# Kernel tuning notes

Hardware: AMD Instinct MI355X
Metric: run time of the kernel (lower is better)

The kernel has to match this reference:

```python
import jax, jax.numpy as jnp
import numpy as np

NUM_EMBEDDINGS = 4096
EMBEDDING_DIM = 256
COMMITMENT_COST = 0.25
N_TOKENS = 32768


def setup_inputs() -> dict:
    key = jax.random.key(0)
    k1, k2 = jax.random.split(key)
    inputs = jax.random.normal(k1, (N_TOKENS, EMBEDDING_DIM), dtype=jnp.float32)
    # torch init: uniform(-1/K, 1/K)
    lim = 1.0 / NUM_EMBEDDINGS
    weight = jax.random.uniform(k2, (NUM_EMBEDDINGS, EMBEDDING_DIM), dtype=jnp.float32,
                                minval=-lim, maxval=lim)
    return {"inputs": inputs, "weight": weight}


def reference(inputs, weight):
    distances = (jnp.sum(inputs ** 2, axis=1, keepdims=True)
                 + jnp.sum(weight ** 2, axis=1)
                 - 2.0 * jnp.matmul(inputs, weight.T))
    encoding_indices = jnp.argmin(distances, axis=1)                       # [N]
    encodings = jax.nn.one_hot(encoding_indices, NUM_EMBEDDINGS,
                               dtype=jnp.float32)                          # [N, K]
    # gather replaces onehot @ weight (same values)
    quantized = weight[encoding_indices]                                   # [N, D]

    commitment_loss = jnp.mean((jax.lax.stop_gradient(quantized) - inputs) ** 2)
    codebook_loss = jnp.mean((quantized - jax.lax.stop_gradient(inputs)) ** 2)
    loss = codebook_loss + COMMITMENT_COST * commitment_loss

    # straight-through estimator
    quantized_st = inputs + jax.lax.stop_gradient(quantized - inputs)

    avg_probs = jnp.mean(encodings, axis=0)                                # [K]
    perplexity = jnp.exp(-jnp.sum(avg_probs * jnp.log(avg_probs + 1e-10)))

    return (quantized_st, perplexity, encodings, encoding_indices, loss)
```

## Files before the change

### kernel.cpp

```cpp
#include <hip/hip_runtime.h>

#define N_TOK 32768
#define N_EMB 4096
#define DIM 256

typedef short bf16x8 __attribute__((ext_vector_type(8)));
typedef float f32x4 __attribute__((ext_vector_type(4)));
typedef unsigned short us8 __attribute__((ext_vector_type(8)));


static __device__ __forceinline__ unsigned short f2bf(float f) {
    unsigned int u = __float_as_uint(f);
    u = (u + 0x7fffu + ((u >> 16) & 1u)) >> 16;
    return (unsigned short)u;
}

__device__ __forceinline__ float pw128_sq(const float4* a4) {
#pragma clang fp contract(off)
    float4 v0 = a4[0], v1 = a4[1];
    float r0 = v0.x * v0.x, r1 = v0.y * v0.y, r2 = v0.z * v0.z, r3 = v0.w * v0.w;
    float r4 = v1.x * v1.x, r5 = v1.y * v1.y, r6 = v1.z * v1.z, r7 = v1.w * v1.w;
    #pragma unroll
    for (int i = 1; i < 16; ++i) {
        v0 = a4[2 * i]; v1 = a4[2 * i + 1];
        float s;
        s = v0.x * v0.x; r0 += s;
        s = v0.y * v0.y; r1 += s;
        s = v0.z * v0.z; r2 += s;
        s = v0.w * v0.w; r3 += s;
        s = v1.x * v1.x; r4 += s;
        s = v1.y * v1.y; r5 += s;
        s = v1.z * v1.z; r6 += s;
        s = v1.w * v1.w; r7 += s;
    }
    return ((r0 + r1) + (r2 + r3)) + ((r4 + r5) + (r6 + r7));
}

__global__ __launch_bounds__(256) void k_norm_np(const float* __restrict__ src,
                                                 float* __restrict__ dst, int nrows) {
#pragma clang fp contract(off)
    int row = blockIdx.x * 256 + threadIdx.x;
    if (row >= nrows) return;
    const float4* a = (const float4*)(src + (size_t)row * DIM);
    float lo = pw128_sq(a);
    float hi = pw128_sq(a + 32);
    dst[row] = lo + hi;
}

__global__ __launch_bounds__(256) void k_shuf1(const float* __restrict__ src,
                                               unsigned short* __restrict__ hi) {
    int tid = blockIdx.x * 256 + threadIdx.x;
    int b = tid >> 6, lane = tid & 63;
    int T = b >> 3, C = b & 7;
    int row = T * 16 + (lane & 15);
    int col = C * 32 + (lane >> 4) * 8;
    const float* s = src + (size_t)row * DIM + col;
    us8 h;
    #pragma unroll
    for (int j = 0; j < 8; ++j) h[j] = f2bf(s[j]);
    *(us8*)(hi + (size_t)tid * 8) = h;
}

__global__ __launch_bounds__(256, 4) void k_score_mfma(
        const float* __restrict__ x, const float* __restrict__ w,
        const float* __restrict__ e2_np, const float* __restrict__ x2_np,
        const unsigned short* __restrict__ Xh,
        const unsigned short* __restrict__ Wh,
        float* __restrict__ out_idx, unsigned int* __restrict__ counts,
        float* enc,
        float* __restrict__ outq, float* __restrict__ loss_acc) {
    __shared__ __align__(16) short Abuf[8192];
    __shared__ float Tmax[4][32];
    __shared__ unsigned int ccnt[32];
    __shared__ int clist[32][16];
    __shared__ float Red_d[32 * 8];
    __shared__ int   Red_i[32 * 8];
    __shared__ float sred[4];

    const int t = threadIdx.x;
    const int wave = t >> 6, lane = t & 63;
    const int tok0 = blockIdx.x * 32;
    const int q = lane >> 4, c = lane & 15;

    #pragma unroll
    for (int i = 0; i < 4; ++i) {
        int idx = wave * 4 + i;
        int tile = idx >> 3, C = idx & 7;
        int Tg = blockIdx.x * 2 + tile;
        const unsigned short* src = Xh + ((size_t)(Tg * 8 + C) * 64 + lane) * 8;
        __builtin_amdgcn_global_load_lds(
            (const __attribute__((address_space(1))) unsigned int*)src,
            (__attribute__((address_space(3))) unsigned int*)(Abuf + idx * 512),
            16, 0, 0);
    }
    if (t < 32) ccnt[t] = 0;
    __syncthreads();

    f32x4* ez = enc ? (f32x4*)(enc + (size_t)tok0 * N_EMB) : (f32x4*)0;
    const f32x4 zf4 = {0.f, 0.f, 0.f, 0.f};

    float vmax[8], v2[8];
    #pragma unroll
    for (int s = 0; s < 8; ++s) { vmax[s] = -3.4e38f; v2[s] = -3.4e38f; }
    for (int jt = 0; jt < N_EMB; jt += 256) {
        const int U0 = (jt >> 4) + wave * 4;
        f32x4 acc[2][4] = {};
        #pragma unroll
        for (int C = 0; C < 8; ++C) {
            bf16x8 ah[2], bh[4];
            #pragma unroll
            for (int m = 0; m < 2; ++m)
                ah[m] = *(const bf16x8*)(Abuf + (size_t)(m * 8 + C) * 512 + lane * 8);
            #pragma unroll
            for (int n = 0; n < 4; ++n)
                bh[n] = *(const bf16x8*)(Wh + (((size_t)(U0 + n) * 8 + C) * 64 + lane) * 8);
            #pragma unroll
            for (int m = 0; m < 2; ++m)
                #pragma unroll
                for (int n = 0; n < 4; ++n)
                    acc[m][n] = __builtin_amdgcn_mfma_f32_16x16x32_bf16(ah[m], bh[n], acc[m][n], 0, 0, 0);
        }
        {
            unsigned int idb = ((unsigned int)jt >> 8) << 2;
            #pragma unroll
            for (int m = 0; m < 2; ++m)
                #pragma unroll
                for (int n = 0; n < 4; ++n)
                    #pragma unroll
                    for (int r = 0; r < 4; ++r) {
                        float p = __uint_as_float(
                            (__float_as_uint(acc[m][n][r]) & ~63u) | (idb + (unsigned)n));
                        int s = m * 4 + r;
                        if (p > vmax[s]) { v2[s] = vmax[s]; vmax[s] = p; }
                        else if (p > v2[s]) v2[s] = p;
                    }
        }
        if (ez) {
            int base = (jt >> 8) * 8 * 256 + t;
            #pragma unroll
            for (int j = 0; j < 8; ++j)
                __builtin_nontemporal_store(zf4, ez + base + j * 256);
        }
    }
    float rmax[8];
    #pragma unroll
    for (int s = 0; s < 8; ++s) rmax[s] = vmax[s];
    #pragma unroll
    for (int off = 1; off < 16; off <<= 1)
        #pragma unroll
        for (int s = 0; s < 8; ++s)
            rmax[s] = fmaxf(rmax[s], __shfl_xor(rmax[s], off));
    if (c == 0) {
        #pragma unroll
        for (int m = 0; m < 2; ++m)
            #pragma unroll
            for (int r = 0; r < 4; ++r)
                Tmax[wave][m * 16 + q * 4 + r] = rmax[m * 4 + r];
    }
    __syncthreads();
    if (t < 32) {
        float mx = fmaxf(fmaxf(Tmax[0][t], Tmax[1][t]),
                         fmaxf(Tmax[2][t], Tmax[3][t]));
        Tmax[0][t] = mx - 1.5e-4f;
    }
    __syncthreads();
    float thr[8];
    #pragma unroll
    for (int m = 0; m < 2; ++m)
        #pragma unroll
        for (int r = 0; r < 4; ++r)
            thr[m * 4 + r] = Tmax[0][m * 16 + q * 4 + r];

    #pragma unroll
    for (int s = 0; s < 8; ++s) {
        int m = s >> 2, r = s & 3;
        int tokl = m * 16 + q * 4 + r;
        #pragma unroll
        for (int h = 0; h < 2; ++h) {
            float pv = h ? v2[s] : vmax[s];
            if (pv >= thr[s]) {
                unsigned int id = __float_as_uint(pv) & 63u;
                int code = ((int)(id >> 2) * 16 + wave * 4 + (int)(id & 3u)) * 16 + c;
                unsigned int p = atomicAdd(&ccnt[tokl], 1u);
                if (p < 16) clist[tokl][p] = code;
            }
        }
    }
    __syncthreads();

    {
        int token = t >> 3, slot = t & 7;
        int cnt = (int)ccnt[token]; if (cnt > 16) cnt = 16;
        float bd = 3.4e38f;
        int bi = 0x7fffffff;
        float x2 = x2_np[tok0 + token];
        const float4* xr = (const float4*)(x + (size_t)(tok0 + token) * DIM);
        for (int k = slot; k < cnt; k += 8) {
            int code = clist[token][k];
            const float4* wr = (const float4*)(w + (size_t)code * DIM);
            double dot = 0.0;
            for (int g = 0; g < 64; ++g) {
                float4 xv = xr[g];
                float4 wv = wr[g];
                dot += (double)xv.x * (double)wv.x;
                dot += (double)xv.y * (double)wv.y;
                dot += (double)xv.z * (double)wv.z;
                dot += (double)xv.w * (double)wv.w;
            }
            {
#pragma clang fp contract(off)
                float M  = (float)dot;
                float S  = x2 + e2_np[code];
                float dd = S - 2.0f * M;
                if (dd < bd || (dd == bd && code < bi)) { bd = dd; bi = code; }
            }
        }
        Red_d[token * 8 + slot] = bd;
        Red_i[token * 8 + slot] = bi;
    }
    __syncthreads();
    if (t < 32) {
        float fv = Red_d[t * 8];
        int   fi = Red_i[t * 8];
        #pragma unroll
        for (int k = 1; k < 8; ++k) {
            float v = Red_d[t * 8 + k];
            int  ii = Red_i[t * 8 + k];
            if (v < fv || (v == fv && ii < fi)) { fv = v; fi = ii; }
        }
        out_idx[tok0 + t] = (float)fi;
        atomicAdd(&counts[fi], 1u);
        ccnt[t] = (unsigned int)fi;
    }
    __syncthreads();

    {
        int token = t >> 3, slot = t & 7;
        int fi = (int)ccnt[token];
        if (enc && slot == 0)
            __builtin_nontemporal_store(1.0f, enc + (size_t)(tok0 + token) * N_EMB + fi);
        const f32x4* wr = (const f32x4*)(w + (size_t)fi * DIM);
        const f32x4* xr = (const f32x4*)(x + (size_t)(tok0 + token) * DIM);
        f32x4* oq = (f32x4*)(outq + (size_t)(tok0 + token) * DIM);
        float sse = 0.f;
        #pragma unroll
        for (int g0 = 0; g0 < 8; ++g0) {
            int g = slot * 8 + g0;
            f32x4 qv = wr[g];
            f32x4 xv = xr[g];
            __builtin_nontemporal_store(qv, oq + g);
            float dx = qv.x - xv.x, dy = qv.y - xv.y;
            float dz = qv.z - xv.z, dw = qv.w - xv.w;
            sse += dx * dx + dy * dy + dz * dz + dw * dw;
        }
        #pragma unroll
        for (int off = 32; off > 0; off >>= 1) sse += __shfl_down(sse, off, 64);
        if (lane == 0) sred[wave] = sse;
    }
    __syncthreads();
    if (t == 0)
        atomicAdd(loss_acc, sred[0] + sred[1] + sred[2] + sred[3]);
}

__global__ __launch_bounds__(256) void k_onehot(const float* __restrict__ out_idx,
                                                float* __restrict__ enc) {
    int token = blockIdx.x;
    int idx = (int)out_idx[token];
    float4* row = (float4*)(enc + (size_t)token * N_EMB);
    #pragma unroll
    for (int p = 0; p < 4; ++p) {
        int g = threadIdx.x + 256 * p;
        float4 v = make_float4(0.f, 0.f, 0.f, 0.f);
        int d0 = g * 4;
        if (idx >= d0 && idx < d0 + 4) ((float*)&v)[idx - d0] = 1.0f;
        row[g] = v;
    }
}

__global__ __launch_bounds__(256) void k_final(const unsigned int* __restrict__ counts,
                                               const float* __restrict__ loss_acc,
                                               float* __restrict__ out_perp,
                                               float* __restrict__ out_loss) {
    __shared__ float sred[4];
    int t = threadIdx.x;
    float h = 0.f;
    for (int k = t; k < N_EMB; k += 256) {
        float p = (float)counts[k] * (1.0f / N_TOK);
        h += p * logf(p + 1e-10f);
    }
    #pragma unroll
    for (int off = 32; off > 0; off >>= 1) h += __shfl_down(h, off, 64);
    if ((t & 63) == 0) sred[t >> 6] = h;
    __syncthreads();
    if (t == 0) {
        float s = sred[0] + sred[1] + sred[2] + sred[3];
        *out_perp = expf(-s);
        *out_loss = loss_acc[0] * 1.25f / 8388608.0f;
    }
}

extern "C" void kernel_launch(void* const* d_in, const int* in_sizes, int n_in,
                              void* d_out, int out_size, void* d_ws, size_t ws_size,
                              hipStream_t stream) {
    const float* x = (const float*)d_in[0];
    const float* w = (const float*)d_in[1];
    float* out  = (float*)d_out;
    float* out0 = out;
    float* out1 = out0 + 8388608;
    float* out2 = out1 + 1;
    float* out3 = out2 + 134217728;
    float* out4 = out3 + 32768;

    unsigned int* counts = (unsigned int*)d_ws;
    float* loss_acc = (float*)((char*)d_ws + 16384);
    float* e2_np    = (float*)((char*)d_ws + 16896);
    float* x2_np    = (float*)((char*)d_ws + 33280);

    bool big_ws = ws_size >= (size_t)(20u * 1024u * 1024u);
    unsigned short *Xh, *Wh;
    float* enc_arg;
    if (big_ws) {
        Xh = (unsigned short*)((char*)d_ws + (1u << 20));
        Wh = Xh + 8388608;
        enc_arg = out2;
    } else {
        uintptr_t sb = ((uintptr_t)out2 + 255) & ~(uintptr_t)255;
        Xh = (unsigned short*)sb;
        Wh = Xh + 8388608;
        enc_arg = nullptr;
    }

    hipMemsetAsync(d_ws, 0, 16640, stream);
    k_norm_np<<<N_EMB / 256, 256, 0, stream>>>(w, e2_np, N_EMB);
    k_norm_np<<<N_TOK / 256, 256, 0, stream>>>(x, x2_np, N_TOK);
    k_shuf1<<<N_TOK * DIM / 8 / 256, 256, 0, stream>>>(x, Xh);
    k_shuf1<<<N_EMB * DIM / 8 / 256, 256, 0, stream>>>(w, Wh);
    k_score_mfma<<<N_TOK / 32, 256, 0, stream>>>(x, w, e2_np, x2_np, Xh, Wh,
                                                 out3, counts, enc_arg,
                                                 out0, loss_acc);
    if (!big_ws)
        k_onehot<<<N_TOK, 256, 0, stream>>>(out3, out2);
    k_final<<<1, 256, 0, stream>>>(counts, loss_acc, out1, out4);
}
```

Measured before the change: 756.5 us.

## Double token tile per block and use branchless top-2 tracking

Each scoring block now handles 64 tokens instead of 32, so every W fragment loaded from global memory feeds four MFMAs instead of two. This halves the total codebook traffic across the grid. The top-2 tracking after each MFMA tile is rewritten with fmax/fmed3 instead of branches, processing four candidates at a time. In exchange the accumulators and top-2 state double, which raises register pressure (launch bounds lowered to 3 waves), halves the grid, and gives fewer threads per token in the refinement and output phases.

```diff
diff --git a/kernel.cpp b/kernel.cpp
--- a/kernel.cpp
+++ b/kernel.cpp
@@ -13,6 +13,10 @@
     unsigned int u = __float_as_uint(f);
     u = (u + 0x7fffu + ((u >> 16) & 1u)) >> 16;
     return (unsigned short)u;
+}
+
+static __device__ __forceinline__ float pkid(float x, unsigned int id) {
+    return __uint_as_float((__float_as_uint(x) & ~63u) | id);
 }
 
 __device__ __forceinline__ float pw128_sq(const float4* a4) {
@@ -61,7 +65,7 @@
     *(us8*)(hi + (size_t)tid * 8) = h;
 }
 
-__global__ __launch_bounds__(256, 4) void k_score_mfma(
+__global__ __launch_bounds__(256, 3) void k_score_mfma(
         const float* __restrict__ x, const float* __restrict__ w,
         const float* __restrict__ e2_np, const float* __restrict__ x2_np,
         const unsigned short* __restrict__ Xh,
@@ -69,110 +73,113 @@
         float* __restrict__ out_idx, unsigned int* __restrict__ counts,
         float* enc,
         float* __restrict__ outq, float* __restrict__ loss_acc) {
-    __shared__ __align__(16) short Abuf[8192];
-    __shared__ float Tmax[4][32];
-    __shared__ unsigned int ccnt[32];
-    __shared__ int clist[32][16];
-    __shared__ float Red_d[32 * 8];
-    __shared__ int   Red_i[32 * 8];
+    __shared__ __align__(16) short Abuf[16384];
+    __shared__ float Tmax[4][64];
+    __shared__ unsigned int ccnt[64];
+    __shared__ int clist[64][16];
+    __shared__ float Red_d[64 * 4];
+    __shared__ int   Red_i[64 * 4];
     __shared__ float sred[4];
 
     const int t = threadIdx.x;
     const int wave = t >> 6, lane = t & 63;
-    const int tok0 = blockIdx.x * 32;
+    const int tok0 = blockIdx.x * 64;
     const int q = lane >> 4, c = lane & 15;
 
     #pragma unroll
-    for (int i = 0; i < 4; ++i) {
-        int idx = wave * 4 + i;
+    for (int i = 0; i < 8; ++i) {
+        int idx = wave * 8 + i;
         int tile = idx >> 3, C = idx & 7;
-        int Tg = blockIdx.x * 2 + tile;
+        int Tg = blockIdx.x * 4 + tile;
         const unsigned short* src = Xh + ((size_t)(Tg * 8 + C) * 64 + lane) * 8;
         __builtin_amdgcn_global_load_lds(
             (const __attribute__((address_space(1))) unsigned int*)src,
             (__attribute__((address_space(3))) unsigned int*)(Abuf + idx * 512),
             16, 0, 0);
     }
-    if (t < 32) ccnt[t] = 0;
+    if (t < 64) ccnt[t] = 0;
     __syncthreads();
 
     f32x4* ez = enc ? (f32x4*)(enc + (size_t)tok0 * N_EMB) : (f32x4*)0;
     const f32x4 zf4 = {0.f, 0.f, 0.f, 0.f};
 
-    float vmax[8], v2[8];
-    #pragma unroll
-    for (int s = 0; s < 8; ++s) { vmax[s] = -3.4e38f; v2[s] = -3.4e38f; }
+    float vmax[16], v2[16];
+    #pragma unroll
+    for (int s = 0; s < 16; ++s) { vmax[s] = -3.4e38f; v2[s] = -3.4e38f; }
     for (int jt = 0; jt < N_EMB; jt += 256) {
         const int U0 = (jt >> 4) + wave * 4;
-        f32x4 acc[2][4] = {};
+        f32x4 acc[4][4] = {};
         #pragma unroll
         for (int C = 0; C < 8; ++C) {
-            bf16x8 ah[2], bh[4];
-            #pragma unroll
-            for (int m = 0; m < 2; ++m)
+            bf16x8 ah[4];
+            #pragma unroll
+            for (int m = 0; m < 4; ++m)
                 ah[m] = *(const bf16x8*)(Abuf + (size_t)(m * 8 + C) * 512 + lane * 8);
             #pragma unroll
-            for (int n = 0; n < 4; ++n)
-                bh[n] = *(const bf16x8*)(Wh + (((size_t)(U0 + n) * 8 + C) * 64 + lane) * 8);
-            #pragma unroll
-            for (int m = 0; m < 2; ++m)
+            for (int n = 0; n < 4; ++n) {
+                bf16x8 bh = *(const bf16x8*)(Wh + (((size_t)(U0 + n) * 8 + C) * 64 + lane) * 8);
                 #pragma unroll
-                for (int n = 0; n < 4; ++n)
-                    acc[m][n] = __builtin_amdgcn_mfma_f32_16x16x32_bf16(ah[m], bh[n], acc[m][n], 0, 0, 0);
+                for (int m = 0; m < 4; ++m)
+                    acc[m][n] = __builtin_amdgcn_mfma_f32_16x16x32_bf16(ah[m], bh, acc[m][n], 0, 0, 0);
+            }
         }
         {
             unsigned int idb = ((unsigned int)jt >> 8) << 2;
             #pragma unroll
-            for (int m = 0; m < 2; ++m)
+            for (int m = 0; m < 4; ++m)
                 #pragma unroll
-                for (int n = 0; n < 4; ++n)
-                    #pragma unroll
-                    for (int r = 0; r < 4; ++r) {
-                        float p = __uint_as_float(
-                            (__float_as_uint(acc[m][n][r]) & ~63u) | (idb + (unsigned)n));
-                        int s = m * 4 + r;
-                        if (p > vmax[s]) { v2[s] = vmax[s]; vmax[s] = p; }
-                        else if (p > v2[s]) v2[s] = p;
-                    }
+                for (int r = 0; r < 4; ++r) {
+                    int s = m * 4 + r;
+                    float p0 = pkid(acc[m][0][r], idb + 0);
+                    float p1 = pkid(acc[m][1][r], idb + 1);
+                    float p2 = pkid(acc[m][2][r], idb + 2);
+                    float p3 = pkid(acc[m][3][r], idb + 3);
+                    float t1a = fmaxf(fmaxf(vmax[s], p0), p1);
+                    float t2a = __builtin_amdgcn_fmed3f(vmax[s], p0, p1);
+                    float t1b = fmaxf(fmaxf(v2[s], p2), p3);
+                    float t2b = __builtin_amdgcn_fmed3f(v2[s], p2, p3);
+                    vmax[s] = fmaxf(t1a, t1b);
+                    v2[s]   = fmaxf(fmaxf(fminf(t1a, t1b), t2a), t2b);
+                }
         }
         if (ez) {
-            int base = (jt >> 8) * 8 * 256 + t;
-            #pragma unroll
-            for (int j = 0; j < 8; ++j)
+            int base = (jt >> 8) * 4096 + t;
+            #pragma unroll
+            for (int j = 0; j < 16; ++j)
                 __builtin_nontemporal_store(zf4, ez + base + j * 256);
         }
     }
-    float rmax[8];
-    #pragma unroll
-    for (int s = 0; s < 8; ++s) rmax[s] = vmax[s];
+    float rmax[16];
+    #pragma unroll
+    for (int s = 0; s < 16; ++s) rmax[s] = vmax[s];
     #pragma unroll
     for (int off = 1; off < 16; off <<= 1)
         #pragma unroll
-        for (int s = 0; s < 8; ++s)
+        for (int s = 0; s < 16; ++s)
             rmax[s] = fmaxf(rmax[s], __shfl_xor(rmax[s], off));
     if (c == 0) {
         #pragma unroll
-        for (int m = 0; m < 2; ++m)
+        for (int m = 0; m < 4; ++m)
             #pragma unroll
             for (int r = 0; r < 4; ++r)
                 Tmax[wave][m * 16 + q * 4 + r] = rmax[m * 4 + r];
     }
     __syncthreads();
-    if (t < 32) {
+    if (t < 64) {
         float mx = fmaxf(fmaxf(Tmax[0][t], Tmax[1][t]),
                          fmaxf(Tmax[2][t], Tmax[3][t]));
         Tmax[0][t] = mx - 1.5e-4f;
     }
     __syncthreads();
-    float thr[8];
-    #pragma unroll
-    for (int m = 0; m < 2; ++m)
+    float thr[16];
+    #pragma unroll
+    for (int m = 0; m < 4; ++m)
         #pragma unroll
         for (int r = 0; r < 4; ++r)
             thr[m * 4 + r] = Tmax[0][m * 16 + q * 4 + r];
 
     #pragma unroll
-    for (int s = 0; s < 8; ++s) {
+    for (int s = 0; s < 16; ++s) {
         int m = s >> 2, r = s & 3;
         int tokl = m * 16 + q * 4 + r;
         #pragma unroll
@@ -189,13 +196,13 @@
     __syncthreads();
 
     {
-        int token = t >> 3, slot = t & 7;
+        int token = t >> 2, slot = t & 3;
         int cnt = (int)ccnt[token]; if (cnt > 16) cnt = 16;
         float bd = 3.4e38f;
         int bi = 0x7fffffff;
         float x2 = x2_np[tok0 + token];
         const float4* xr = (const float4*)(x + (size_t)(tok0 + token) * DIM);
-        for (int k = slot; k < cnt; k += 8) {
+        for (int k = slot; k < cnt; k += 4) {
             int code = clist[token][k];
             const float4* wr = (const float4*)(w + (size_t)code * DIM);
             double dot = 0.0;
@@ -215,17 +222,17 @@
                 if (dd < bd || (dd == bd && code < bi)) { bd = dd; bi = code; }
             }
         }
-        Red_d[token * 8 + slot] = bd;
-        Red_i[token * 8 + slot] = bi;
-    }
-    __syncthreads();
-    if (t < 32) {
-        float fv = Red_d[t * 8];
-        int   fi = Red_i[t * 8];
-        #pragma unroll
-        for (int k = 1; k < 8; ++k) {
-            float v = Red_d[t * 8 + k];
-            int  ii = Red_i[t * 8 + k];
+        Red_d[token * 4 + slot] = bd;
+        Red_i[token * 4 + slot] = bi;
+    }
+    __syncthreads();
+    if (t < 64) {
+        float fv = Red_d[t * 4];
+        int   fi = Red_i[t * 4];
+        #pragma unroll
+        for (int k = 1; k < 4; ++k) {
+            float v = Red_d[t * 4 + k];
+            int  ii = Red_i[t * 4 + k];
             if (v < fv || (v == fv && ii < fi)) { fv = v; fi = ii; }
         }
         out_idx[tok0 + t] = (float)fi;
@@ -235,7 +242,7 @@
     __syncthreads();
 
     {
-        int token = t >> 3, slot = t & 7;
+        int token = t >> 2, slot = t & 3;
         int fi = (int)ccnt[token];
         if (enc && slot == 0)
             __builtin_nontemporal_store(1.0f, enc + (size_t)(tok0 + token) * N_EMB + fi);
@@ -244,8 +251,8 @@
         f32x4* oq = (f32x4*)(outq + (size_t)(tok0 + token) * DIM);
         float sse = 0.f;
         #pragma unroll
-        for (int g0 = 0; g0 < 8; ++g0) {
-            int g = slot * 8 + g0;
+        for (int g0 = 0; g0 < 16; ++g0) {
+            int g = slot * 16 + g0;
             f32x4 qv = wr[g];
             f32x4 xv = xr[g];
             __builtin_nontemporal_store(qv, oq + g);
@@ -335,7 +342,7 @@
     k_norm_np<<<N_TOK / 256, 256, 0, stream>>>(x, x2_np, N_TOK);
     k_shuf1<<<N_TOK * DIM / 8 / 256, 256, 0, stream>>>(x, Xh);
     k_shuf1<<<N_EMB * DIM / 8 / 256, 256, 0, stream>>>(w, Wh);
-    k_score_mfma<<<N_TOK / 32, 256, 0, stream>>>(x, w, e2_np, x2_np, Xh, Wh,
+    k_score_mfma<<<N_TOK / 64, 256, 0, stream>>>(x, w, e2_np, x2_np, Xh, Wh,
                                                  out3, counts, enc_arg,
                                                  out0, loss_acc);
     if (!big_ws)
```

Measured after the change: 881.1 us. 1.16x slower.
